# Performance work log

Hardware: AMD Instinct MI355X
Metric: run time of the kernel (lower is better)

Reference implementation:

```python
import jax, jax.numpy as jnp
import numpy as np

B, N, C = 8, 4096, 768
H = 12
D = C // H  # 64


def setup_inputs() -> dict:
    key = jax.random.key(0)
    k1, k2, k3 = jax.random.split(key, 3)
    x = jax.random.normal(k1, (B, N, C), dtype=jnp.float32)
    Wqkv = jax.random.normal(k2, (C, 3 * C), dtype=jnp.float32) * (1.0 / np.sqrt(C))
    Wproj = jax.random.normal(k3, (C, C), dtype=jnp.float32) * (1.0 / np.sqrt(C))
    bproj = jnp.zeros((C,), dtype=jnp.float32)
    return {"x": x, "Wqkv": Wqkv, "Wproj": Wproj, "bproj": bproj}


def reference(x, Wqkv, Wproj, bproj):
    b, n, c = x.shape
    # qkv: [B,N,3C] -> [B,N,3,H,D] -> [3,B,H,N,D]
    qkv = (x @ Wqkv).reshape(b, n, 3, H, D).transpose(2, 0, 3, 1, 4)
    q, k, v = qkv[0], qkv[1], qkv[2]
    q = jax.nn.softmax(q, axis=-1)  # softmax over head_dim (feature map)
    k = jax.nn.softmax(k, axis=-1)
    # context: [B,H,D,D] (small per-head matrix)
    context = jnp.einsum('bhnd,bhne->bhde', k, v)
    out = jnp.einsum('bhnd,bhde->bhne', q, context)  # [B,H,N,D]
    out = out.transpose(0, 2, 1, 3).reshape(b, n, c)
    return out @ Wproj + bproj
```

## Files before the change

### kernel.cpp

```cpp
#include <hip/hip_runtime.h>

typedef unsigned short u16;
typedef unsigned int u32;
typedef __attribute__((ext_vector_type(4))) float f32x4;
typedef __attribute__((ext_vector_type(8))) short bf16x8;
typedef __attribute__((ext_vector_type(8))) u16 u16x8;

__device__ __forceinline__ u16 f2b(float f) {
  union { float f; u32 u; } v; v.f = f;
  u32 r = v.u + 0x7FFFu + ((v.u >> 16) & 1u);
  return (u16)(r >> 16);
}
__device__ __forceinline__ float b2f(u16 h) {
  union { u32 u; float f; } v; v.u = ((u32)h) << 16;
  return v.f;
}
__device__ __forceinline__ void gload_lds16(const void* g, void* lds) {
  __builtin_amdgcn_global_load_lds(
      (__attribute__((address_space(1))) void*)(void*)g,
      (__attribute__((address_space(3))) void*)lds, 16, 0, 0);
}

__global__ __launch_bounds__(256) void cast_x_kernel(const float* __restrict__ x,
                                                     u16* __restrict__ xb, size_t n8) {
  size_t i = (size_t)blockIdx.x * blockDim.x + threadIdx.x;
  size_t stride = (size_t)gridDim.x * blockDim.x;
  for (; i < n8; i += stride) {
    const float4* p = (const float4*)(x + i * 8);
    float4 a = p[0], b = p[1];
    u16x8 o;
    o[0] = f2b(a.x); o[1] = f2b(a.y); o[2] = f2b(a.z); o[3] = f2b(a.w);
    o[4] = f2b(b.x); o[5] = f2b(b.y); o[6] = f2b(b.z); o[7] = f2b(b.w);
    *(u16x8*)(xb + i * 8) = o;
  }
}

__global__ __launch_bounds__(256) void transpose_cast_kernel(const float* __restrict__ W,
                                                             u16* __restrict__ WT,
                                                             int R, int C) {
  __shared__ u16 tile[32][33];
  int rt = R >> 5;
  int tr = blockIdx.x % rt, tc = blockIdx.x / rt;
  int r0 = tr * 32, c0 = tc * 32;
#pragma unroll
  for (int i = 0; i < 4; ++i) {
    int r = (threadIdx.x >> 5) + i * 8, c = threadIdx.x & 31;
    tile[r][c] = f2b(W[(size_t)(r0 + r) * C + c0 + c]);
  }
  __syncthreads();
#pragma unroll
  for (int i = 0; i < 4; ++i) {
    int c = (threadIdx.x >> 5) + i * 8, r = threadIdx.x & 31;
    WT[(size_t)(c0 + c) * R + r0 + r] = tile[r][c];
  }
}

template <bool OUT_BF16, bool BIAS, bool SOFTMAX, bool BATCHB>
__global__ __launch_bounds__(256, 4) void gemm128_kernel(
    const u16* __restrict__ A, const u16* __restrict__ BT, void* __restrict__ Cv,
    const float* __restrict__ bias, int N, int lda, int ntile) {
  constexpr int K = 768;
  constexpr int NT = 24;
  __shared__ __align__(16) u16 As[2 * 4096];
  __shared__ __align__(16) u16 Bs[3 * 4096];
  const int tid = threadIdx.x;
  const int wave = tid >> 6, lane = tid & 63;
  const int lr = lane & 15, hi = lane >> 4;
  const int wr = wave >> 1, wc = wave & 1;

  const int cpx = gridDim.x >> 3;
  const int wg = (blockIdx.x & 7) * cpx + (blockIdx.x >> 3);
  const int tm = wg / ntile, tn = wg % ntile;

  const size_t rowA0 = (size_t)tm * 128;
  const size_t rowB0 = (size_t)tn * 128;
  const u16* BTb = BATCHB ? (BT + (size_t)(tm >> 5) * 589824) : BT;

  const int dby = tid * 16;
  const int sby = dby ^ (((dby >> 7) & 3) << 4);
  const int srow = sby >> 6;
  const int scol = (sby & 63) >> 1;
  const u16* pA = A + (rowA0 + srow) * (size_t)lda + scol;
  const u16* pB = BTb + (rowB0 + srow) * (size_t)K + scol;
  u16* Adst = As + wave * 512;
  u16* Bdst = Bs + wave * 512;

  const int flip = ((lr >> 1) & 3) << 4;
  const int baseA = ((((wr * 64 + lr) * 64) + hi * 16) ^ flip) >> 1;
  const int baseB = ((((wc * 64 + lr) * 64) + hi * 16) ^ flip) >> 1;

  f32x4 acc[4][4] = {};

#define STG_A(tt)                                                          \
  { const u16* _s = pA + (size_t)(tt) * 32;                                \
    u16* _d = Adst + ((tt) & 1) * 4096;                                    \
    gload_lds16(_s, _d); gload_lds16(_s + (size_t)64 * lda, _d + 2048); }
#define STG_B(tt)                                                          \
  { const u16* _s = pB + (size_t)(tt) * 32;                                \
    u16* _d = Bdst + ((tt) % 3) * 4096;                                    \
    gload_lds16(_s, _d); gload_lds16(_s + (size_t)64 * K, _d + 2048); }

  STG_A(0); STG_B(0); STG_B(1);
  asm volatile("s_waitcnt vmcnt(2)" ::: "memory");
  __builtin_amdgcn_sched_barrier(0);
  __builtin_amdgcn_s_barrier();

#pragma unroll
  for (int t = 0; t < NT; ++t) {
    const u16* Ab = As + (t & 1) * 4096;
    const u16* Bb = Bs + (t % 3) * 4096;
    bf16x8 a0 = *(const bf16x8*)&Ab[baseA];
    bf16x8 a1 = *(const bf16x8*)&Ab[baseA + 512];
    bf16x8 a2 = *(const bf16x8*)&Ab[baseA + 1024];
    bf16x8 a3 = *(const bf16x8*)&Ab[baseA + 1536];
    bf16x8 b0 = *(const bf16x8*)&Bb[baseB];
    bf16x8 b1 = *(const bf16x8*)&Bb[baseB + 512];
    bf16x8 b2 = *(const bf16x8*)&Bb[baseB + 1024];
    bf16x8 b3 = *(const bf16x8*)&Bb[baseB + 1536];
    if (t + 1 < NT) STG_A(t + 1);
    if (t + 2 < NT) STG_B(t + 2);
    __builtin_amdgcn_s_barrier();
    asm volatile("s_waitcnt lgkmcnt(0)" ::: "memory");
    __builtin_amdgcn_sched_barrier(0);
    __builtin_amdgcn_s_setprio(1);
    acc[0][0] = __builtin_amdgcn_mfma_f32_16x16x32_bf16(a0, b0, acc[0][0], 0, 0, 0);
    acc[0][1] = __builtin_amdgcn_mfma_f32_16x16x32_bf16(a0, b1, acc[0][1], 0, 0, 0);
    acc[0][2] = __builtin_amdgcn_mfma_f32_16x16x32_bf16(a0, b2, acc[0][2], 0, 0, 0);
    acc[0][3] = __builtin_amdgcn_mfma_f32_16x16x32_bf16(a0, b3, acc[0][3], 0, 0, 0);
    acc[1][0] = __builtin_amdgcn_mfma_f32_16x16x32_bf16(a1, b0, acc[1][0], 0, 0, 0);
    acc[1][1] = __builtin_amdgcn_mfma_f32_16x16x32_bf16(a1, b1, acc[1][1], 0, 0, 0);
    acc[1][2] = __builtin_amdgcn_mfma_f32_16x16x32_bf16(a1, b2, acc[1][2], 0, 0, 0);
    acc[1][3] = __builtin_amdgcn_mfma_f32_16x16x32_bf16(a1, b3, acc[1][3], 0, 0, 0);
    acc[2][0] = __builtin_amdgcn_mfma_f32_16x16x32_bf16(a2, b0, acc[2][0], 0, 0, 0);
    acc[2][1] = __builtin_amdgcn_mfma_f32_16x16x32_bf16(a2, b1, acc[2][1], 0, 0, 0);
    acc[2][2] = __builtin_amdgcn_mfma_f32_16x16x32_bf16(a2, b2, acc[2][2], 0, 0, 0);
    acc[2][3] = __builtin_amdgcn_mfma_f32_16x16x32_bf16(a2, b3, acc[2][3], 0, 0, 0);
    acc[3][0] = __builtin_amdgcn_mfma_f32_16x16x32_bf16(a3, b0, acc[3][0], 0, 0, 0);
    acc[3][1] = __builtin_amdgcn_mfma_f32_16x16x32_bf16(a3, b1, acc[3][1], 0, 0, 0);
    acc[3][2] = __builtin_amdgcn_mfma_f32_16x16x32_bf16(a3, b2, acc[3][2], 0, 0, 0);
    acc[3][3] = __builtin_amdgcn_mfma_f32_16x16x32_bf16(a3, b3, acc[3][3], 0, 0, 0);
    __builtin_amdgcn_s_setprio(0);
    if (t < NT - 2) {
      asm volatile("s_waitcnt vmcnt(2)" ::: "memory");
    } else if (t == NT - 2) {
      asm volatile("s_waitcnt vmcnt(0)" ::: "memory");
    }
    __builtin_amdgcn_sched_barrier(0);
    if (t + 1 < NT) __builtin_amdgcn_s_barrier();
  }
#undef STG_A
#undef STG_B

  const int ocol0 = tn * 128 + wc * 64;
  const int orow0 = tm * 128 + wr * 64;
  const bool do_sm = SOFTMAX && (ocol0 < 1536);
#pragma unroll
  for (int mf = 0; mf < 4; ++mf) {
    if (do_sm) {
#pragma unroll
      for (int q = 0; q < 4; ++q) {
        float v0 = acc[mf][0][q], v1 = acc[mf][1][q];
        float v2 = acc[mf][2][q], v3 = acc[mf][3][q];
        float mx = fmaxf(fmaxf(v0, v1), fmaxf(v2, v3));
#pragma unroll
        for (int s = 1; s <= 8; s <<= 1) mx = fmaxf(mx, __shfl_xor(mx, s, 64));
        float e0 = __expf(v0 - mx), e1 = __expf(v1 - mx);
        float e2 = __expf(v2 - mx), e3 = __expf(v3 - mx);
        float sm = e0 + e1 + e2 + e3;
#pragma unroll
        for (int s = 1; s <= 8; s <<= 1) sm += __shfl_xor(sm, s, 64);
        float inv = 1.0f / sm;
        acc[mf][0][q] = e0 * inv; acc[mf][1][q] = e1 * inv;
        acc[mf][2][q] = e2 * inv; acc[mf][3][q] = e3 * inv;
      }
    }
#pragma unroll
    for (int nf = 0; nf < 4; ++nf) {
      const int col = ocol0 + nf * 16 + lr;
      const float bv = BIAS ? bias[col] : 0.0f;
#pragma unroll
      for (int q = 0; q < 4; ++q) {
        const int row = orow0 + mf * 16 + hi * 4 + q;
        const float v = acc[mf][nf][q] + bv;
        if (OUT_BF16) ((u16*)Cv)[(size_t)row * N + col] = f2b(v);
        else          ((float*)Cv)[(size_t)row * N + col] = v;
      }
    }
  }
}

#define NS 8
__global__ __launch_bounds__(256) void ctx_partial_kernel(const u16* __restrict__ qkv,
                                                          float* __restrict__ partial) {
  __shared__ u16 kT[64 * 136];
  __shared__ u16 vT[64 * 136];
  int bh = blockIdx.x / NS, sp = blockIdx.x % NS;
  int b = bh / 12, h = bh % 12;
  int tid = threadIdx.x, wave = tid >> 6, lane = tid & 63;
  int lr = lane & 15, lk = (lane >> 4) << 3;
  f32x4 acc[4] = {};
  int baseK = 768 + h * 64, baseV = 1536 + h * 64;

  for (int sub = 0; sub < 4; ++sub) {
    int nbase = b * 4096 + sp * 512 + sub * 128;
    __syncthreads();
#pragma unroll
    for (int it = 0; it < 4; ++it) {
      int s = it * 256 + tid;
      int n = s >> 3, c8 = (s & 7) * 8;
      u16x8 kv = *(const u16x8*)(qkv + (size_t)(nbase + n) * 2304 + baseK + c8);
      u16x8 vv = *(const u16x8*)(qkv + (size_t)(nbase + n) * 2304 + baseV + c8);
#pragma unroll
      for (int q = 0; q < 8; ++q) {
        kT[(c8 + q) * 136 + n] = kv[q];
        vT[(c8 + q) * 136 + n] = vv[q];
      }
    }
    __syncthreads();
#pragma unroll
    for (int ks = 0; ks < 4; ++ks) {
      bf16x8 af = *(const bf16x8*)&kT[(wave * 16 + lr) * 136 + ks * 32 + lk];
#pragma unroll
      for (int jt = 0; jt < 4; ++jt) {
        bf16x8 bfv = *(const bf16x8*)&vT[(jt * 16 + lr) * 136 + ks * 32 + lk];
        acc[jt] = __builtin_amdgcn_mfma_f32_16x16x32_bf16(af, bfv, acc[jt], 0, 0, 0);
      }
    }
  }
  float* dst = partial + ((size_t)sp * 96 + bh) * 4096;
#pragma unroll
  for (int jt = 0; jt < 4; ++jt)
#pragma unroll
    for (int q = 0; q < 4; ++q) {
      int d = wave * 16 + (lane >> 4) * 4 + q;
      int e = jt * 16 + lr;
      dst[d * 64 + e] = acc[jt][q];
    }
}

__global__ __launch_bounds__(256) void ctx_reduce_kernel(const float* __restrict__ partial,
                                                         u16* __restrict__ ctxD) {
  int idx = blockIdx.x * 256 + threadIdx.x;
  int bh = idx >> 12;
  int de = idx & 4095;
  float s = 0.0f;
#pragma unroll
  for (int sp = 0; sp < NS; ++sp) s += partial[((size_t)sp * 96 + bh) * 4096 + de];
  ctxD[(size_t)bh * 4096 + de] = f2b(s);
}

__global__ __launch_bounds__(256) void make_w2_kernel(const u16* __restrict__ WprojT,
                                                      const u16* __restrict__ ctxD,
                                                      u16* __restrict__ BT2) {
  __shared__ u16 qs[128 * 64];
  __shared__ u16 cs[64 * 64];
  int bid = blockIdx.x;
  int b = bid / 72, rest = bid % 72;
  int h = rest / 6, ct = rest % 6;
  int bh = b * 12 + h;
  int tid = threadIdx.x, wave = tid >> 6, lane = tid & 63;
  int lr = lane & 15, lk = (lane >> 4) << 3;
#pragma unroll
  for (int it = 0; it < 4; ++it) {
    int u = it * 256 + tid;
    int r = u >> 3, c8 = (u & 7) * 8;
    gload_lds16(WprojT + (size_t)(ct * 128 + r) * 768 + h * 64 + c8,
                &qs[(it * 256 + wave * 64) * 8]);
  }
#pragma unroll
  for (int it = 0; it < 2; ++it) {
    int u = it * 256 + tid;
    gload_lds16(ctxD + (size_t)bh * 4096 + u * 8, &cs[(it * 256 + wave * 64) * 8]);
  }
  asm volatile("s_waitcnt vmcnt(0)" ::: "memory");
  __syncthreads();
  f32x4 acc[2][4] = {};
#pragma unroll
  for (int ks = 0; ks < 2; ++ks) {
    bf16x8 bv[4];
#pragma unroll
    for (int jt = 0; jt < 4; ++jt) bv[jt] = *(const bf16x8*)&cs[(jt * 16 + lr) * 64 + ks * 32 + lk];
#pragma unroll
    for (int i = 0; i < 2; ++i) {
      bf16x8 af = *(const bf16x8*)&qs[(wave * 32 + i * 16 + lr) * 64 + ks * 32 + lk];
#pragma unroll
      for (int jt = 0; jt < 4; ++jt)
        acc[i][jt] = __builtin_amdgcn_mfma_f32_16x16x32_bf16(af, bv[jt], acc[i][jt], 0, 0, 0);
    }
  }
#pragma unroll
  for (int i = 0; i < 2; ++i)
#pragma unroll
    for (int jt = 0; jt < 4; ++jt)
#pragma unroll
      for (int q = 0; q < 4; ++q) {
        int cp = ct * 128 + wave * 32 + i * 16 + (lane >> 4) * 4 + q;
        int col = h * 64 + jt * 16 + lr;
        BT2[(size_t)b * 589824 + (size_t)cp * 768 + col] = f2b(acc[i][jt][q]);
      }
}

extern "C" void kernel_launch(void* const* d_in, const int* in_sizes, int n_in,
                              void* d_out, int out_size, void* d_ws, size_t ws_size,
                              hipStream_t stream) {
  const float* x = (const float*)d_in[0];
  const float* Wqkv = (const float*)d_in[1];
  const float* Wproj = (const float*)d_in[2];
  const float* bproj = (const float*)d_in[3];
  float* out = (float*)d_out;
  char* ws = (char*)d_ws;

  u16* xb      = (u16*)(ws);
  u16* WqkvT   = (u16*)(ws + 50331648);
  u16* WprojT  = (u16*)(ws + 53870592);
  u16* qkv     = (u16*)(ws + 55050240);
  float* partial = (float*)(ws + 206045184);
  u16* ctxD    = (u16*)(ws + 218628096);
  u16* BT2     = (u16*)(ws + 219414528);

  cast_x_kernel<<<2048, 256, 0, stream>>>(x, xb, (size_t)(32768ll * 768 / 8));
  transpose_cast_kernel<<<(768 / 32) * (2304 / 32), 256, 0, stream>>>(Wqkv, WqkvT, 768, 2304);
  transpose_cast_kernel<<<(768 / 32) * (768 / 32), 256, 0, stream>>>(Wproj, WprojT, 768, 768);

  gemm128_kernel<true, false, true, false><<<(32768 / 128) * (2304 / 128), 256, 0, stream>>>(
      xb, WqkvT, (void*)qkv, nullptr, 2304, 768, 2304 / 128);

  ctx_partial_kernel<<<96 * NS, 256, 0, stream>>>(qkv, partial);
  ctx_reduce_kernel<<<(96 * 4096) / 256, 256, 0, stream>>>(partial, ctxD);
  make_w2_kernel<<<8 * 12 * 6, 256, 0, stream>>>(WprojT, ctxD, BT2);

  gemm128_kernel<false, true, false, true><<<(32768 / 128) * (768 / 128), 256, 0, stream>>>(
      qkv, BT2, (void*)out, bproj, 768, 2304, 768 / 128);
}
```

Before: 292.6 us.

## Split QKV output into Q and interleaved per-head KV buffers; drop a barrier

The QKV GEMM now writes Q into its own contiguous [N,768] buffer and K/V into a separate [N,1536] buffer with K and V interleaved per head. The Wqkv columns are permuted when the weight is transposed to produce that order. The context kernel reads K and V from adjacent 128-column regions, and the projection GEMM reads Q with a stride of 768 instead of 2304, so its loads waste less bandwidth. A workgroup barrier before the LDS wait in the GEMM main loop is also removed, which risks a read/write race on the LDS buffers.

Measured after the change: 294.4 us. About the same (+0.6%).

```diff
diff --git a/kernel.cpp b/kernel.cpp
--- a/kernel.cpp
+++ b/kernel.cpp
@@ -35,6 +35,7 @@
   }
 }
 
+template <bool PERM>
 __global__ __launch_bounds__(256) void transpose_cast_kernel(const float* __restrict__ W,
                                                              u16* __restrict__ WT,
                                                              int R, int C) {
@@ -51,14 +52,21 @@
 #pragma unroll
   for (int i = 0; i < 4; ++i) {
     int c = (threadIdx.x >> 5) + i * 8, r = threadIdx.x & 31;
-    WT[(size_t)(c0 + c) * R + r0 + r] = tile[r][c];
-  }
-}
-
-template <bool OUT_BF16, bool BIAS, bool SOFTMAX, bool BATCHB>
+    int cc = c0 + c;
+    if (PERM && cc >= 768) {
+      int t = cc - 768;
+      int isv = (t >= 768) ? 1 : 0;
+      int tk = t - isv * 768;
+      cc = 768 + (tk >> 6) * 128 + isv * 64 + (tk & 63);
+    }
+    WT[(size_t)cc * R + r0 + r] = tile[r][c];
+  }
+}
+
+template <bool OUT_BF16, bool BIAS, bool SOFTMAX, bool BATCHB, bool SPLIT>
 __global__ __launch_bounds__(256, 4) void gemm128_kernel(
     const u16* __restrict__ A, const u16* __restrict__ BT, void* __restrict__ Cv,
-    const float* __restrict__ bias, int N, int lda, int ntile) {
+    void* __restrict__ Cv2, const float* __restrict__ bias, int N, int lda, int ntile) {
   constexpr int K = 768;
   constexpr int NT = 24;
   __shared__ __align__(16) u16 As[2 * 4096];
@@ -119,7 +127,6 @@
     bf16x8 b3 = *(const bf16x8*)&Bb[baseB + 1536];
     if (t + 1 < NT) STG_A(t + 1);
     if (t + 2 < NT) STG_B(t + 2);
-    __builtin_amdgcn_s_barrier();
     asm volatile("s_waitcnt lgkmcnt(0)" ::: "memory");
     __builtin_amdgcn_sched_barrier(0);
     __builtin_amdgcn_s_setprio(1);
@@ -153,7 +160,8 @@
 
   const int ocol0 = tn * 128 + wc * 64;
   const int orow0 = tm * 128 + wr * 64;
-  const bool do_sm = SOFTMAX && (ocol0 < 1536);
+  const bool do_sm = SOFTMAX && (SPLIT ? (ocol0 < 768 || (ocol0 & 64) == 0)
+                                       : (ocol0 < 1536));
 #pragma unroll
   for (int mf = 0; mf < 4; ++mf) {
     if (do_sm) {
@@ -182,15 +190,21 @@
       for (int q = 0; q < 4; ++q) {
         const int row = orow0 + mf * 16 + hi * 4 + q;
         const float v = acc[mf][nf][q] + bv;
-        if (OUT_BF16) ((u16*)Cv)[(size_t)row * N + col] = f2b(v);
-        else          ((float*)Cv)[(size_t)row * N + col] = v;
+        if (SPLIT) {
+          if (ocol0 < 768) ((u16*)Cv)[(size_t)row * 768 + col] = f2b(v);
+          else             ((u16*)Cv2)[(size_t)row * 1536 + (col - 768)] = f2b(v);
+        } else if (OUT_BF16) {
+          ((u16*)Cv)[(size_t)row * N + col] = f2b(v);
+        } else {
+          ((float*)Cv)[(size_t)row * N + col] = v;
+        }
       }
     }
   }
 }
 
 #define NS 8
-__global__ __launch_bounds__(256) void ctx_partial_kernel(const u16* __restrict__ qkv,
+__global__ __launch_bounds__(256) void ctx_partial_kernel(const u16* __restrict__ kvbuf,
                                                           float* __restrict__ partial) {
   __shared__ u16 kT[64 * 136];
   __shared__ u16 vT[64 * 136];
@@ -199,7 +213,7 @@
   int tid = threadIdx.x, wave = tid >> 6, lane = tid & 63;
   int lr = lane & 15, lk = (lane >> 4) << 3;
   f32x4 acc[4] = {};
-  int baseK = 768 + h * 64, baseV = 1536 + h * 64;
+  int baseK = h * 128, baseV = h * 128 + 64;
 
   for (int sub = 0; sub < 4; ++sub) {
     int nbase = b * 4096 + sp * 512 + sub * 128;
@@ -208,8 +222,8 @@
     for (int it = 0; it < 4; ++it) {
       int s = it * 256 + tid;
       int n = s >> 3, c8 = (s & 7) * 8;
-      u16x8 kv = *(const u16x8*)(qkv + (size_t)(nbase + n) * 2304 + baseK + c8);
-      u16x8 vv = *(const u16x8*)(qkv + (size_t)(nbase + n) * 2304 + baseV + c8);
+      u16x8 kv = *(const u16x8*)(kvbuf + (size_t)(nbase + n) * 1536 + baseK + c8);
+      u16x8 vv = *(const u16x8*)(kvbuf + (size_t)(nbase + n) * 1536 + baseV + c8);
 #pragma unroll
       for (int q = 0; q < 8; ++q) {
         kT[(c8 + q) * 136 + n] = kv[q];
@@ -313,22 +327,23 @@
   u16* xb      = (u16*)(ws);
   u16* WqkvT   = (u16*)(ws + 50331648);
   u16* WprojT  = (u16*)(ws + 53870592);
-  u16* qkv     = (u16*)(ws + 55050240);
+  u16* qbuf    = (u16*)(ws + 55050240);
+  u16* kvbuf   = (u16*)(ws + 105381888);
   float* partial = (float*)(ws + 206045184);
   u16* ctxD    = (u16*)(ws + 218628096);
   u16* BT2     = (u16*)(ws + 219414528);
 
   cast_x_kernel<<<2048, 256, 0, stream>>>(x, xb, (size_t)(32768ll * 768 / 8));
-  transpose_cast_kernel<<<(768 / 32) * (2304 / 32), 256, 0, stream>>>(Wqkv, WqkvT, 768, 2304);
-  transpose_cast_kernel<<<(768 / 32) * (768 / 32), 256, 0, stream>>>(Wproj, WprojT, 768, 768);
-
-  gemm128_kernel<true, false, true, false><<<(32768 / 128) * (2304 / 128), 256, 0, stream>>>(
-      xb, WqkvT, (void*)qkv, nullptr, 2304, 768, 2304 / 128);
-
-  ctx_partial_kernel<<<96 * NS, 256, 0, stream>>>(qkv, partial);
+  transpose_cast_kernel<true><<<(768 / 32) * (2304 / 32), 256, 0, stream>>>(Wqkv, WqkvT, 768, 2304);
+  transpose_cast_kernel<false><<<(768 / 32) * (768 / 32), 256, 0, stream>>>(Wproj, WprojT, 768, 768);
+
+  gemm128_kernel<true, false, true, false, true><<<(32768 / 128) * (2304 / 128), 256, 0, stream>>>(
+      xb, WqkvT, (void*)qbuf, (void*)kvbuf, nullptr, 2304, 768, 2304 / 128);
+
+  ctx_partial_kernel<<<96 * NS, 256, 0, stream>>>(kvbuf, partial);
   ctx_reduce_kernel<<<(96 * 4096) / 256, 256, 0, stream>>>(partial, ctxD);
   make_w2_kernel<<<8 * 12 * 6, 256, 0, stream>>>(WprojT, ctxD, BT2);
 
-  gemm128_kernel<false, true, false, true><<<(32768 / 128) * (768 / 128), 256, 0, stream>>>(
-      qkv, BT2, (void*)out, bproj, 768, 2304, 768 / 128);
-}
+  gemm128_kernel<false, true, false, true, false><<<(32768 / 128) * (768 / 128), 256, 0, stream>>>(
+      qbuf, BT2, (void*)out, nullptr, bproj, 768, 768, 768 / 128);
+}
```
